# Optimization experiments

Hardware: AMD Instinct MI355X
Metric: run time of the kernel (lower is better)

Reference implementation:

```python
import jax, jax.numpy as jnp
import numpy as np

NX, NY, C, B, P = 432, 496, 64, 4, 40000


def setup_inputs() -> dict:
    key = jax.random.key(0)
    k1, _ = jax.random.split(key)
    pillar_features = jax.random.normal(k1, (P, C), dtype=jnp.float32)
    # Build voxel_coords with unique (x, y) cells per batch element so the
    # scatter-write has no duplicate indices (matches deterministic torch assignment).
    rng = np.random.default_rng(0)
    per = P // B  # pillars per sample
    coords = np.empty((P, 3), dtype=np.int64)
    for b in range(B):
        flat = rng.choice(NX * NY, size=per, replace=False)
        coords[b * per:(b + 1) * per, 0] = flat % NX          # x index
        coords[b * per:(b + 1) * per, 1] = flat // NX         # y index
        coords[b * per:(b + 1) * per, 2] = b                  # batch index (last col)
    return {
        "pillar_features": pillar_features,
        "voxel_coords": jnp.asarray(coords),
        "batch_size": B,
        "nx": NX,
        "ny": NY,
    }


def reference(pillar_features, voxel_coords, batch_size, nx, ny):
    # Fused scatter: compute a global flat index (batch, y, x) for every pillar
    # and scatter all pillars in a single pass (no per-batch masking loop).
    x = voxel_coords[:, 0]
    y = voxel_coords[:, 1]
    b = voxel_coords[:, -1]
    flat = b * (ny * nx) + y * nx + x                       # [P]
    c = pillar_features.shape[1]
    grid = jnp.zeros((batch_size * ny * nx, c), dtype=pillar_features.dtype)
    grid = grid.at[flat].set(pillar_features)               # scatter pillars
    # [B*ny*nx, C] -> [B, C, ny, nx]
    return grid.reshape(batch_size, ny, nx, c).transpose(0, 3, 1, 2)
```

## Files before the change

kernel.cpp:

```cpp
#include <hip/hip_runtime.h>


#define C_CH 64

__global__ void build_map_kernel(const int* __restrict__ coords, int n_pillars,
                                 const int* __restrict__ nx_p,
                                 const int* __restrict__ ny_p,
                                 int* __restrict__ map) {
    int p = blockIdx.x * blockDim.x + threadIdx.x;
    if (p >= n_pillars) return;
    const int nx = nx_p[0];
    const int ny = ny_p[0];
    const int x = coords[3 * p + 0];
    const int y = coords[3 * p + 1];
    const int b = coords[3 * p + 2];
    const long long m = (long long)b * (long long)(nx * ny) + (long long)y * nx + x;
    map[m] = p;
}

__global__ void gather64_kernel(const float* __restrict__ feat,
                                const int* __restrict__ map,
                                const int* __restrict__ nx_p,
                                const int* __restrict__ ny_p,
                                float* __restrict__ out, int n_map) {
    const int tid = blockIdx.x * blockDim.x + threadIdx.x;
    if (tid >= n_map) return;
    const int plane = nx_p[0] * ny_p[0];
    const int b = tid / plane;
    const int rem = tid - b * plane;
    const size_t base = (size_t)b * C_CH * (size_t)plane + (size_t)rem;

    const int p = map[tid];

    float vals[C_CH];
#pragma unroll
    for (int c = 0; c < C_CH; ++c) vals[c] = 0.0f;

    if (p >= 0) {
        const float4* __restrict__ src =
            (const float4*)(feat + (size_t)p * C_CH);
#pragma unroll
        for (int i = 0; i < C_CH / 4; ++i) {
            float4 v = src[i];
            vals[4 * i + 0] = v.x;
            vals[4 * i + 1] = v.y;
            vals[4 * i + 2] = v.z;
            vals[4 * i + 3] = v.w;
        }
    }

#pragma unroll
    for (int c = 0; c < C_CH; ++c) {
        out[base + (size_t)c * (size_t)plane] = vals[c];
    }
}

__global__ void direct_scatter_kernel(const float* __restrict__ feat,
                                      const int* __restrict__ coords,
                                      int n_pillars, int C,
                                      const int* __restrict__ nx_p,
                                      const int* __restrict__ ny_p,
                                      float* __restrict__ out) {
    const long long t = (long long)blockIdx.x * blockDim.x + threadIdx.x;
    if (t >= (long long)n_pillars * C) return;
    const int p = (int)(t / C);
    const int c = (int)(t - (long long)p * C);
    const int nx = nx_p[0];
    const int ny = ny_p[0];
    const int x = coords[3 * p + 0];
    const int y = coords[3 * p + 1];
    const int b = coords[3 * p + 2];
    const int plane = nx * ny;
    const size_t o = ((size_t)b * C + c) * (size_t)plane + (size_t)y * nx + x;
    out[o] = feat[(size_t)p * C + c];
}

extern "C" void kernel_launch(void* const* d_in, const int* in_sizes, int n_in,
                              void* d_out, int out_size, void* d_ws, size_t ws_size,
                              hipStream_t stream) {
    const float* feat   = (const float*)d_in[0];
    const int*   coords = (const int*)d_in[1];
    const int* nx_p = (const int*)d_in[3];
    const int* ny_p = (const int*)d_in[4];
    float* out = (float*)d_out;

    const int n_pillars = in_sizes[1] / 3;
    const int C = in_sizes[0] / n_pillars;
    const int n_map = out_size / C;
    const size_t map_bytes = (size_t)n_map * sizeof(int);

    if (C == C_CH && ws_size >= map_bytes) {
        int* map = (int*)d_ws;
        hipMemsetAsync(map, 0xFF, map_bytes, stream);
        build_map_kernel<<<(n_pillars + 255) / 256, 256, 0, stream>>>(
            coords, n_pillars, nx_p, ny_p, map);
        gather64_kernel<<<(n_map + 255) / 256, 256, 0, stream>>>(
            feat, map, nx_p, ny_p, out, n_map);
    } else {
        hipMemsetAsync(out, 0, (size_t)out_size * sizeof(float), stream);
        const long long total = (long long)n_pillars * C;
        direct_scatter_kernel<<<(unsigned)((total + 255) / 256), 256, 0, stream>>>(
            feat, coords, n_pillars, C, nx_p, ny_p, out);
    }
}
```

Baseline: 232.7 us.

## Restructure gather to per-channel grid with float4 vectorized output writes

Replaces the one-thread-per-cell gather, which loaded 64 channels and wrote 64 strided scalars, with a 2D grid where each thread handles four consecutive cells for one channel and writes one float4. This makes output stores wide and fully coalesced. The cost is that the map is re-read once per channel (64 times) and feature reads become scattered 4-byte loads with a stride of C, though most cells are empty and those are mostly served from cache.

```diff
diff --git a/kernel.cpp b/kernel.cpp
--- a/kernel.cpp
+++ b/kernel.cpp
@@ -18,40 +18,40 @@
     map[m] = p;
 }
 
-__global__ void gather64_kernel(const float* __restrict__ feat,
-                                const int* __restrict__ map,
-                                const int* __restrict__ nx_p,
-                                const int* __restrict__ ny_p,
-                                float* __restrict__ out, int n_map) {
-    const int tid = blockIdx.x * blockDim.x + threadIdx.x;
-    if (tid >= n_map) return;
+__global__ void gather_c4_kernel(const float* __restrict__ feat,
+                                 const int* __restrict__ map,
+                                 const int* __restrict__ nx_p,
+                                 const int* __restrict__ ny_p,
+                                 float* __restrict__ out, int n_map) {
+    const int c = blockIdx.y;
+    const int cell = (blockIdx.x * blockDim.x + threadIdx.x) * 4;
+    if (cell >= n_map) return;
     const int plane = nx_p[0] * ny_p[0];
-    const int b = tid / plane;
-    const int rem = tid - b * plane;
-    const size_t base = (size_t)b * C_CH * (size_t)plane + (size_t)rem;
 
-    const int p = map[tid];
+    if ((plane & 3) == 0) {
+        const int4 m = *reinterpret_cast<const int4*>(map + cell);
+        const unsigned b = (unsigned)cell / (unsigned)plane;
+        const int local = cell - (int)b * plane;
 
-    float vals[C_CH];
+        float4 v;
+        v.x = (m.x >= 0) ? feat[(size_t)m.x * C_CH + c] : 0.0f;
+        v.y = (m.y >= 0) ? feat[(size_t)m.y * C_CH + c] : 0.0f;
+        v.z = (m.z >= 0) ? feat[(size_t)m.z * C_CH + c] : 0.0f;
+        v.w = (m.w >= 0) ? feat[(size_t)m.w * C_CH + c] : 0.0f;
+
+        *reinterpret_cast<float4*>(
+            out + ((size_t)b * C_CH + c) * (size_t)plane + local) = v;
+    } else {
 #pragma unroll
-    for (int c = 0; c < C_CH; ++c) vals[c] = 0.0f;
-
-    if (p >= 0) {
-        const float4* __restrict__ src =
-            (const float4*)(feat + (size_t)p * C_CH);
-#pragma unroll
-        for (int i = 0; i < C_CH / 4; ++i) {
-            float4 v = src[i];
-            vals[4 * i + 0] = v.x;
-            vals[4 * i + 1] = v.y;
-            vals[4 * i + 2] = v.z;
-            vals[4 * i + 3] = v.w;
+        for (int i = 0; i < 4; ++i) {
+            const int cl = cell + i;
+            if (cl >= n_map) break;
+            const int b = cl / plane;
+            const int local = cl - b * plane;
+            const int p = map[cl];
+            out[((size_t)b * C_CH + c) * (size_t)plane + local] =
+                (p >= 0) ? feat[(size_t)p * C_CH + c] : 0.0f;
         }
-    }
-
-#pragma unroll
-    for (int c = 0; c < C_CH; ++c) {
-        out[base + (size_t)c * (size_t)plane] = vals[c];
     }
 }
 
@@ -94,7 +94,10 @@
         hipMemsetAsync(map, 0xFF, map_bytes, stream);
         build_map_kernel<<<(n_pillars + 255) / 256, 256, 0, stream>>>(
             coords, n_pillars, nx_p, ny_p, map);
-        gather64_kernel<<<(n_map + 255) / 256, 256, 0, stream>>>(
+
+        const int n_quads = (n_map + 3) / 4;
+        dim3 grid((n_quads + 255) / 256, C_CH, 1);
+        gather_c4_kernel<<<grid, 256, 0, stream>>>(
             feat, map, nx_p, ny_p, out, n_map);
     } else {
         hipMemsetAsync(out, 0, (size_t)out_size * sizeof(float), stream);
```

Measured after the change: 288.0 us. 1.24x slower.

## Tile gather through LDS with vectorized nontemporal channel-plane stores

Applied to the files above, without the earlier changes.

Replaces the one-thread-per-cell gather with a block-tiled kernel. Each block handles 1024 cells and stages 16 channels at a time in LDS, then writes each channel plane as contiguous float4 nontemporal stores. The aim is to replace the previous scalar per-channel stores with wider stores and to cut register pressure from the 64-value array. In exchange it adds LDS traffic, two barriers per pass, and a slow scalar fallback for tiles that cross a batch boundary.

```diff
diff --git a/kernel.cpp b/kernel.cpp
--- a/kernel.cpp
+++ b/kernel.cpp
@@ -2,6 +2,12 @@
 
 
 #define C_CH 64
+#define CELLS 1024
+#define CH_PASS 16
+#define NPASS (C_CH / CH_PASS)
+#define BLOCK 256
+
+typedef float fvec4 __attribute__((ext_vector_type(4)));
 
 __global__ void build_map_kernel(const int* __restrict__ coords, int n_pillars,
                                  const int* __restrict__ nx_p,
@@ -18,40 +24,85 @@
     map[m] = p;
 }
 
-__global__ void gather64_kernel(const float* __restrict__ feat,
-                                const int* __restrict__ map,
-                                const int* __restrict__ nx_p,
-                                const int* __restrict__ ny_p,
-                                float* __restrict__ out, int n_map) {
-    const int tid = blockIdx.x * blockDim.x + threadIdx.x;
-    if (tid >= n_map) return;
+__global__ __launch_bounds__(BLOCK, 2) void gather_tile_kernel(
+    const float* __restrict__ feat, const int* __restrict__ map,
+    const int* __restrict__ nx_p, const int* __restrict__ ny_p,
+    float* __restrict__ out, int n_map) {
+    __shared__ float lds[CH_PASS][CELLS];
+
+    const int t = threadIdx.x;
+    const int w = t >> 6;
+    const int l = t & 63;
+    const int cl_base = blockIdx.x * CELLS;
     const int plane = nx_p[0] * ny_p[0];
-    const int b = tid / plane;
-    const int rem = tid - b * plane;
-    const size_t base = (size_t)b * C_CH * (size_t)plane + (size_t)rem;
 
-    const int p = map[tid];
-
-    float vals[C_CH];
+    int pidx[4];
 #pragma unroll
-    for (int c = 0; c < C_CH; ++c) vals[c] = 0.0f;
-
-    if (p >= 0) {
-        const float4* __restrict__ src =
-            (const float4*)(feat + (size_t)p * C_CH);
-#pragma unroll
-        for (int i = 0; i < C_CH / 4; ++i) {
-            float4 v = src[i];
-            vals[4 * i + 0] = v.x;
-            vals[4 * i + 1] = v.y;
-            vals[4 * i + 2] = v.z;
-            vals[4 * i + 3] = v.w;
-        }
+    for (int j = 0; j < 4; ++j) {
+        const int cl = cl_base + t + BLOCK * j;
+        pidx[j] = (cl < n_map) ? map[cl] : -1;
     }
 
+    const int b0 = cl_base / plane;
+    const int local0 = cl_base - b0 * plane;
+    const bool fast = ((plane & 3) == 0) && (cl_base + CELLS <= n_map) &&
+                      ((cl_base + CELLS - 1) / plane == b0);
+
+    for (int cg = 0; cg < NPASS; ++cg) {
 #pragma unroll
-    for (int c = 0; c < C_CH; ++c) {
-        out[base + (size_t)c * (size_t)plane] = vals[c];
+        for (int j = 0; j < 4; ++j) {
+            const int pos = t + BLOCK * j;
+            const int p = pidx[j];
+            float vals[CH_PASS];
+            if (p >= 0) {
+                const float4* __restrict__ src =
+                    (const float4*)(feat + (size_t)p * C_CH + cg * CH_PASS);
+#pragma unroll
+                for (int q = 0; q < CH_PASS / 4; ++q) {
+                    const float4 v = src[q];
+                    vals[4 * q + 0] = v.x;
+                    vals[4 * q + 1] = v.y;
+                    vals[4 * q + 2] = v.z;
+                    vals[4 * q + 3] = v.w;
+                }
+            } else {
+#pragma unroll
+                for (int q = 0; q < CH_PASS; ++q) vals[q] = 0.0f;
+            }
+#pragma unroll
+            for (int q = 0; q < CH_PASS; ++q) lds[q][pos] = vals[q];
+        }
+        __syncthreads();
+
+#pragma unroll
+        for (int pl = 0; pl < 4; ++pl) {
+            const int cc = 4 * w + pl;
+            const int c = cg * CH_PASS + cc;
+            if (fast) {
+                fvec4* __restrict__ dst =
+                    (fvec4*)(out + ((size_t)(b0 * C_CH + c)) * (size_t)plane +
+                             local0);
+                const fvec4* __restrict__ src = (const fvec4*)&lds[cc][0];
+#pragma unroll
+                for (int k = 0; k < CELLS / 256; ++k) {
+                    __builtin_nontemporal_store(src[64 * k + l], &dst[64 * k + l]);
+                }
+            } else {
+                for (int k = 0; k < CELLS / 256; ++k) {
+                    for (int e = 0; e < 4; ++e) {
+                        const int off = 256 * k + 4 * l + e;
+                        const int cell = cl_base + off;
+                        if (cell < n_map) {
+                            const int b = cell / plane;
+                            const int local = cell - b * plane;
+                            out[((size_t)(b * C_CH + c)) * (size_t)plane + local] =
+                                lds[cc][off];
+                        }
+                    }
+                }
+            }
+        }
+        __syncthreads();
     }
 }
 
@@ -91,13 +142,15 @@
 
     if (C == C_CH && ws_size >= map_bytes) {
         int* map = (int*)d_ws;
-        hipMemsetAsync(map, 0xFF, map_bytes, stream);
+        (void)hipMemsetAsync(map, 0xFF, map_bytes, stream);
         build_map_kernel<<<(n_pillars + 255) / 256, 256, 0, stream>>>(
             coords, n_pillars, nx_p, ny_p, map);
-        gather64_kernel<<<(n_map + 255) / 256, 256, 0, stream>>>(
+
+        const int n_tiles = (n_map + CELLS - 1) / CELLS;
+        gather_tile_kernel<<<n_tiles, BLOCK, 0, stream>>>(
             feat, map, nx_p, ny_p, out, n_map);
     } else {
-        hipMemsetAsync(out, 0, (size_t)out_size * sizeof(float), stream);
+        (void)hipMemsetAsync(out, 0, (size_t)out_size * sizeof(float), stream);
         const long long total = (long long)n_pillars * C;
         direct_scatter_kernel<<<(unsigned)((total + 255) / 256), 256, 0, stream>>>(
             feat, coords, n_pillars, C, nx_p, ny_p, out);
```

Result: slower. 254.8 us (+9.5%).

## Replace map-build and dense gather with memset plus direct per-element scatter

Applied to the files above, without the earlier changes.

Drops the workspace index map and the dense gather kernel that read a map entry and wrote all channels for every grid cell. Instead the output is zero-filled with a bulk memset, and a single kernel scatters each pillar feature element to its channel-planar location, with a shift/mask fast path for 64 channels. This trades the gather's per-cell map lookups and register-heavy writes for a bandwidth-friendly memset plus sparse, uncoalesced scattered writes.

```diff
diff --git a/kernel.cpp b/kernel.cpp
--- a/kernel.cpp
+++ b/kernel.cpp
@@ -1,78 +1,36 @@
 #include <hip/hip_runtime.h>
 
 
-#define C_CH 64
+__global__ void scatter_kernel(const float* __restrict__ feat,
+                               const int* __restrict__ coords,
+                               int n_pillars, int C,
+                               const int* __restrict__ nx_p,
+                               const int* __restrict__ ny_p,
+                               float* __restrict__ out) {
+    const long long t = (long long)blockIdx.x * blockDim.x + threadIdx.x;
+    if (t >= (long long)n_pillars * C) return;
 
-__global__ void build_map_kernel(const int* __restrict__ coords, int n_pillars,
-                                 const int* __restrict__ nx_p,
-                                 const int* __restrict__ ny_p,
-                                 int* __restrict__ map) {
-    int p = blockIdx.x * blockDim.x + threadIdx.x;
-    if (p >= n_pillars) return;
+    int p, c;
+    if (C == 64) {
+        p = (int)(t >> 6);
+        c = (int)(t & 63);
+    } else {
+        p = (int)(t / C);
+        c = (int)(t - (long long)p * C);
+    }
+
     const int nx = nx_p[0];
     const int ny = ny_p[0];
+    const int plane = nx * ny;
+
     const int x = coords[3 * p + 0];
     const int y = coords[3 * p + 1];
     const int b = coords[3 * p + 2];
-    const long long m = (long long)b * (long long)(nx * ny) + (long long)y * nx + x;
-    map[m] = p;
-}
 
-__global__ void gather64_kernel(const float* __restrict__ feat,
-                                const int* __restrict__ map,
-                                const int* __restrict__ nx_p,
-                                const int* __restrict__ ny_p,
-                                float* __restrict__ out, int n_map) {
-    const int tid = blockIdx.x * blockDim.x + threadIdx.x;
-    if (tid >= n_map) return;
-    const int plane = nx_p[0] * ny_p[0];
-    const int b = tid / plane;
-    const int rem = tid - b * plane;
-    const size_t base = (size_t)b * C_CH * (size_t)plane + (size_t)rem;
+    const float v = feat[t];
 
-    const int p = map[tid];
-
-    float vals[C_CH];
-#pragma unroll
-    for (int c = 0; c < C_CH; ++c) vals[c] = 0.0f;
-
-    if (p >= 0) {
-        const float4* __restrict__ src =
-            (const float4*)(feat + (size_t)p * C_CH);
-#pragma unroll
-        for (int i = 0; i < C_CH / 4; ++i) {
-            float4 v = src[i];
-            vals[4 * i + 0] = v.x;
-            vals[4 * i + 1] = v.y;
-            vals[4 * i + 2] = v.z;
-            vals[4 * i + 3] = v.w;
-        }
-    }
-
-#pragma unroll
-    for (int c = 0; c < C_CH; ++c) {
-        out[base + (size_t)c * (size_t)plane] = vals[c];
-    }
-}
-
-__global__ void direct_scatter_kernel(const float* __restrict__ feat,
-                                      const int* __restrict__ coords,
-                                      int n_pillars, int C,
-                                      const int* __restrict__ nx_p,
-                                      const int* __restrict__ ny_p,
-                                      float* __restrict__ out) {
-    const long long t = (long long)blockIdx.x * blockDim.x + threadIdx.x;
-    if (t >= (long long)n_pillars * C) return;
-    const int p = (int)(t / C);
-    const int c = (int)(t - (long long)p * C);
-    const int nx = nx_p[0];
-    const int ny = ny_p[0];
-    const int x = coords[3 * p + 0];
-    const int y = coords[3 * p + 1];
-    const int b = coords[3 * p + 2];
-    const int plane = nx * ny;
     const size_t o = ((size_t)b * C + c) * (size_t)plane + (size_t)y * nx + x;
-    out[o] = feat[(size_t)p * C + c];
+    out[o] = v;
 }
 
 extern "C" void kernel_launch(void* const* d_in, const int* in_sizes, int n_in,
@@ -86,20 +44,11 @@
 
     const int n_pillars = in_sizes[1] / 3;
     const int C = in_sizes[0] / n_pillars;
-    const int n_map = out_size / C;
-    const size_t map_bytes = (size_t)n_map * sizeof(int);
 
-    if (C == C_CH && ws_size >= map_bytes) {
-        int* map = (int*)d_ws;
-        hipMemsetAsync(map, 0xFF, map_bytes, stream);
-        build_map_kernel<<<(n_pillars + 255) / 256, 256, 0, stream>>>(
-            coords, n_pillars, nx_p, ny_p, map);
-        gather64_kernel<<<(n_map + 255) / 256, 256, 0, stream>>>(
-            feat, map, nx_p, ny_p, out, n_map);
-    } else {
-        hipMemsetAsync(out, 0, (size_t)out_size * sizeof(float), stream);
-        const long long total = (long long)n_pillars * C;
-        direct_scatter_kernel<<<(unsigned)((total + 255) / 256), 256, 0, stream>>>(
-            feat, coords, n_pillars, C, nx_p, ny_p, out);
-    }
+    (void)hipMemsetAsync(out, 0, (size_t)out_size * sizeof(float), stream);
+
+    const long long total = (long long)n_pillars * C;
+    const unsigned nblocks = (unsigned)((total + 255) / 256);
+    scatter_kernel<<<nblocks, 256, 0, stream>>>(
+        feat, coords, n_pillars, C, nx_p, ny_p, out);
 }
```

Result: slower. 252.5 us (+8.5%).
